# Optimization experiments

Measured on AMD Instinct MI355X. Metric: run time of the kernel, lower is better.

The kernel has to match this reference:

```python
import jax, jax.numpy as jnp
import numpy as np

DIM = 128
CODEBOOK_SCALE = 16384
N_TOKENS = 16384


def setup_inputs() -> dict:
    key = jax.random.key(0)
    k1, k2 = jax.random.split(key)
    x = jax.random.normal(k1, (N_TOKENS, DIM), dtype=jnp.float32)
    codebook = jax.random.normal(k2, (CODEBOOK_SCALE, DIM), dtype=jnp.float32)
    return {"x": x, "codebook": codebook}


def reference(x, codebook):
    # scores: [N, codebook_scale] = x @ codebook.T
    scores = jnp.einsum("nd,cd->nc", x, codebook)
    indices = jnp.argmax(scores, axis=-1)  # [N] int
    loss = jnp.zeros((), dtype=jnp.float32)  # original returns constant 0.0 loss
    return (indices, loss)
```

## Files before the change

kernel.cpp:

```cpp
#include <hip/hip_runtime.h>
#include <hip/hip_bf16.h>

#define NT 16384
#define ND 128
#define NC 16384
#define NSPLIT 8
#define MARGIN 0.4f
#define TILE_BYTES 16384
#define NTILES 32

typedef __bf16 bf16x8 __attribute__((ext_vector_type(8)));
typedef unsigned short u16x8 __attribute__((ext_vector_type(8)));
typedef float f32x4 __attribute__((ext_vector_type(4)));

#define MF __builtin_amdgcn_mfma_f32_16x16x32_bf16

static __device__ __forceinline__ unsigned short f2bf(float f) {
    unsigned u = __float_as_uint(f);
    return (unsigned short)((u + 0x7FFFu + ((u >> 16) & 1u)) >> 16);
}
static __device__ __forceinline__ float bf2f(unsigned short u) {
    return __uint_as_float(((unsigned)u) << 16);
}
static __device__ __forceinline__ bf16x8 u2b(u16x8 u) {
    return __builtin_bit_cast(bf16x8, u);
}
static __device__ __forceinline__ void gl2lds(const void* g, void* l) {
    __builtin_amdgcn_global_load_lds(
        (const __attribute__((address_space(1))) unsigned int*)g,
        (__attribute__((address_space(3))) unsigned int*)l, 16, 0, 0);
}

__global__ __launch_bounds__(512) void lfq_convert_cb(
    const float4* __restrict__ cb4, unsigned short* __restrict__ cbs)
{
    const unsigned i = blockIdx.x * 512 + threadIdx.x;
    float4 v = cb4[i];
    const unsigned c    = i >> 5;
    const unsigned d0   = (i & 31u) << 2;
    const unsigned tile = c >> 6, r = c & 63u;
    const unsigned pos  = ((d0 >> 3) + r) & 15u;
    const unsigned base = tile * 8192u + r * 128u + pos * 8u + (d0 & 7u);
    ushort4 h;
    h.x = f2bf(v.x);
    h.y = f2bf(v.y);
    h.z = f2bf(v.z);
    h.w = f2bf(v.w);
    *(ushort4*)(cbs + base) = h;
}

static __device__ __forceinline__ float exact_dot(
    const float4* __restrict__ xr4, const float* __restrict__ cf, int cidx)
{
    const float4* cr = (const float4*)(cf + (size_t)cidx * ND);
    float a0 = 0.f, a1 = 0.f, a2 = 0.f, a3 = 0.f;
#pragma unroll
    for (int i = 0; i < 32; i += 4) {
        float4 x0 = xr4[i+0], x1 = xr4[i+1], x2 = xr4[i+2], x3 = xr4[i+3];
        float4 c0 = cr[i+0],  c1 = cr[i+1],  c2 = cr[i+2],  c3 = cr[i+3];
        a0 += x0.x*c0.x + x0.y*c0.y + x0.z*c0.z + x0.w*c0.w;
        a1 += x1.x*c1.x + x1.y*c1.y + x1.z*c1.z + x1.w*c1.w;
        a2 += x2.x*c2.x + x2.y*c2.y + x2.z*c2.z + x2.w*c2.w;
        a3 += x3.x*c3.x + x3.y*c3.y + x3.z*c3.z + x3.w*c3.w;
    }
    return (a0 + a1) + (a2 + a3);
}

static __device__ __forceinline__ float exact_dot_g(
    const float* __restrict__ xf, const float* __restrict__ cf,
    int token, int cidx)
{
    const float4* xr = (const float4*)(xf + (size_t)token * ND);
    const float4* cr = (const float4*)(cf + (size_t)cidx * ND);
    float a0 = 0.f, a1 = 0.f, a2 = 0.f, a3 = 0.f;
#pragma unroll
    for (int i = 0; i < 32; i += 4) {
        float4 x0 = xr[i+0], x1 = xr[i+1], x2 = xr[i+2], x3 = xr[i+3];
        float4 c0 = cr[i+0], c1 = cr[i+1], c2 = cr[i+2], c3 = cr[i+3];
        a0 += x0.x*c0.x + x0.y*c0.y + x0.z*c0.z + x0.w*c0.w;
        a1 += x1.x*c1.x + x1.y*c1.y + x1.z*c1.z + x1.w*c1.w;
        a2 += x2.x*c2.x + x2.y*c2.y + x2.z*c2.z + x2.w*c2.w;
        a3 += x3.x*c3.x + x3.y*c3.y + x3.z*c3.z + x3.w*c3.w;
    }
    return (a0 + a1) + (a2 + a3);
}

static __device__ __forceinline__ void top2_upd(
    const f32x4& a, float* b1r, float* b2r, unsigned pk)
{
#pragma unroll
    for (int r4 = 0; r4 < 4; ++r4) {
        float p = __uint_as_float((__float_as_uint(a[r4]) & 0xFFFFFF80u) | pk);
        b2r[r4] = __builtin_amdgcn_fmed3f(p, b1r[r4], b2r[r4]);
        b1r[r4] = fmaxf(p, b1r[r4]);
    }
}

__global__ __launch_bounds__(256, 4) void lfq_stage1(
    const float* __restrict__ xf, const unsigned short* __restrict__ cbs,
    float* __restrict__ sb1, float* __restrict__ sb2,
    int* __restrict__ si1, int* __restrict__ si2)
{
    const int split = blockIdx.x & 7;
    const int tb    = blockIdx.x >> 3;
    const int t0    = tb * 128;
    const int tid   = threadIdx.x;
    const int w     = tid >> 6;
    const int lane  = tid & 63;
    const int n     = lane & 15;
    const int quad  = lane >> 4;

    __shared__ __attribute__((aligned(16))) unsigned char lds[2 * TILE_BYTES];

    bf16x8 ah[2][4];
#pragma unroll
    for (int tt = 0; tt < 2; ++tt) {
        const float* xr = xf + (size_t)(t0 + w * 32 + tt * 16 + n) * ND + quad * 8;
#pragma unroll
        for (int kk = 0; kk < 4; ++kk) {
            float4 v0 = *(const float4*)(xr + kk * 32);
            float4 v1 = *(const float4*)(xr + kk * 32 + 4);
            u16x8 hu;
            hu[0] = f2bf(v0.x);
            hu[1] = f2bf(v0.y);
            hu[2] = f2bf(v0.z);
            hu[3] = f2bf(v0.w);
            hu[4] = f2bf(v1.x);
            hu[5] = f2bf(v1.y);
            hu[6] = f2bf(v1.z);
            hu[7] = f2bf(v1.w);
            ah[tt][kk] = u2b(hu);
        }
    }

    float b1[2][4], b2[2][4];
#pragma unroll
    for (int tt = 0; tt < 2; ++tt)
#pragma unroll
        for (int r = 0; r < 4; ++r) { b1[tt][r] = -3.0e38f; b2[tt][r] = -3.0e38f; }

    const unsigned char* gtiles =
        (const unsigned char*)cbs + (size_t)(split * NTILES) * TILE_BYTES;
    const unsigned sgo  = (unsigned)(tid * 16);
    const unsigned ldso = (unsigned)(w * 1024);

    const unsigned bb0 = (unsigned)n * 256u + ((((unsigned)(quad + n     )) & 15u) << 4);
    const unsigned bb1 = (unsigned)n * 256u + ((((unsigned)(quad + n +  4)) & 15u) << 4);
    const unsigned bb2 = (unsigned)n * 256u + ((((unsigned)(quad + n +  8)) & 15u) << 4);
    const unsigned bb3 = (unsigned)n * 256u + ((((unsigned)(quad + n + 12)) & 15u) << 4);

    const f32x4 zq = {0.f, 0.f, 0.f, 0.f};

#pragma unroll
    for (int rd = 0; rd < 4; ++rd)
        gl2lds(gtiles + rd * 4096 + sgo, &lds[rd * 4096 + ldso]);
    __syncthreads();

#define PAIR(BUFO, SOFF, PKBASE)                                               \
    {                                                                          \
        bf16x8 qa0 = *(const bf16x8*)&lds[(BUFO) + (SOFF)          + bb0];     \
        bf16x8 qa1 = *(const bf16x8*)&lds[(BUFO) + (SOFF)          + bb1];     \
        bf16x8 qa2 = *(const bf16x8*)&lds[(BUFO) + (SOFF)          + bb2];     \
        bf16x8 qa3 = *(const bf16x8*)&lds[(BUFO) + (SOFF)          + bb3];     \
        bf16x8 qb0 = *(const bf16x8*)&lds[(BUFO) + (SOFF) + 4096u  + bb0];     \
        bf16x8 qb1 = *(const bf16x8*)&lds[(BUFO) + (SOFF) + 4096u  + bb1];     \
        bf16x8 qb2 = *(const bf16x8*)&lds[(BUFO) + (SOFF) + 4096u  + bb2];     \
        bf16x8 qb3 = *(const bf16x8*)&lds[(BUFO) + (SOFF) + 4096u  + bb3];     \
        f32x4 aA0, aA1, aB0, aB1;                                              \
        __builtin_amdgcn_s_setprio(1);                                         \
        aA0 = MF(ah[0][0], qa0, zq,  0,0,0);                                   \
        aA1 = MF(ah[1][0], qa0, zq,  0,0,0);                                   \
        aB0 = MF(ah[0][0], qb0, zq,  0,0,0);                                   \
        aB1 = MF(ah[1][0], qb0, zq,  0,0,0);                                   \
        aA0 = MF(ah[0][1], qa1, aA0, 0,0,0);                                   \
        aA1 = MF(ah[1][1], qa1, aA1, 0,0,0);                                   \
        aB0 = MF(ah[0][1], qb1, aB0, 0,0,0);                                   \
        aB1 = MF(ah[1][1], qb1, aB1, 0,0,0);                                   \
        aA0 = MF(ah[0][2], qa2, aA0, 0,0,0);                                   \
        aA1 = MF(ah[1][2], qa2, aA1, 0,0,0);                                   \
        aB0 = MF(ah[0][2], qb2, aB0, 0,0,0);                                   \
        aB1 = MF(ah[1][2], qb2, aB1, 0,0,0);                                   \
        aA0 = MF(ah[0][3], qa3, aA0, 0,0,0);                                   \
        aA1 = MF(ah[1][3], qa3, aA1, 0,0,0);                                   \
        aB0 = MF(ah[0][3], qb3, aB0, 0,0,0);                                   \
        aB1 = MF(ah[1][3], qb3, aB1, 0,0,0);                                   \
        __builtin_amdgcn_s_setprio(0);                                         \
        const unsigned pkA = (unsigned)(127 - (PKBASE));                       \
        const unsigned pkB = (unsigned)(127 - ((PKBASE) + 1));                 \
        top2_upd(aA0, b1[0], b2[0], pkA);                                      \
        top2_upd(aA1, b1[1], b2[1], pkA);                                      \
        top2_upd(aB0, b1[0], b2[0], pkB);                                      \
        top2_upd(aB1, b1[1], b2[1], pkB);                                      \
    }

#define TILE_BODY(T, BUFO, NBO, PREF)                                          \
    {                                                                          \
        if (PREF) {                                                            \
            const unsigned char* g = gtiles + (size_t)((T) + 1) * TILE_BYTES;  \
            gl2lds(g +     0 + sgo, &lds[(NBO)          + ldso]);              \
            gl2lds(g +  4096 + sgo, &lds[(NBO) +  4096u + ldso]);              \
            gl2lds(g +  8192 + sgo, &lds[(NBO) +  8192u + ldso]);              \
            gl2lds(g + 12288 + sgo, &lds[(NBO) + 12288u + ldso]);              \
        }                                                                      \
        PAIR(BUFO, 0u,    (T) * 4)                                             \
        PAIR(BUFO, 8192u, (T) * 4 + 2)                                         \
    }

    for (int t = 0; t < NTILES; t += 2) {
        TILE_BODY(t,     0u,         TILE_BYTES, 1)
        __syncthreads();
        TILE_BODY(t + 1, TILE_BYTES, 0u,         (t + 2 < NTILES))
        __syncthreads();
    }
#undef TILE_BODY
#undef PAIR

    const int cb_base = split * (NC / NSPLIT);
    float v1[2][4], v2[2][4];
    int   c1[2][4], c2[2][4];
#pragma unroll
    for (int tt = 0; tt < 2; ++tt)
#pragma unroll
        for (int r = 0; r < 4; ++r) {
            int j1 = 127 - (int)(__float_as_uint(b1[tt][r]) & 127u);
            int j2 = 127 - (int)(__float_as_uint(b2[tt][r]) & 127u);
            v1[tt][r] = b1[tt][r]; c1[tt][r] = cb_base + j1 * 16 + n;
            v2[tt][r] = b2[tt][r]; c2[tt][r] = cb_base + j2 * 16 + n;
        }

#pragma unroll
    for (int tt = 0; tt < 2; ++tt)
#pragma unroll
        for (int r = 0; r < 4; ++r) {
#pragma unroll
            for (int off = 1; off < 16; off <<= 1) {
                float ob1 = __shfl_xor(v1[tt][r], off, 64);
                int   oi1 = __shfl_xor(c1[tt][r], off, 64);
                float ob2 = __shfl_xor(v2[tt][r], off, 64);
                int   oi2 = __shfl_xor(c2[tt][r], off, 64);
                bool gt = (ob1 > v1[tt][r]) ||
                          (ob1 == v1[tt][r] && oi1 < c1[tt][r]);
                float ls = gt ? v1[tt][r] : ob1;
                int   li = gt ? c1[tt][r] : oi1;
                float ws_ = gt ? ob2 : v2[tt][r];
                int   wi = gt ? oi2 : c2[tt][r];
                bool s2 = (ls > ws_) || (ls == ws_ && li < wi);
                v2[tt][r] = s2 ? ls : ws_;
                c2[tt][r] = s2 ? li : wi;
                v1[tt][r] = gt ? ob1 : v1[tt][r];
                c1[tt][r] = gt ? oi1 : c1[tt][r];
            }
        }

    if (n == 0) {
#pragma unroll
        for (int tt = 0; tt < 2; ++tt)
#pragma unroll
            for (int r = 0; r < 4; ++r) {
                const int token = t0 + w * 32 + tt * 16 + quad * 4 + r;
                const size_t o = (size_t)split * NT + token;
                sb1[o] = v1[tt][r]; si1[o] = c1[tt][r];
                sb2[o] = v2[tt][r]; si2[o] = c2[tt][r];
            }
    }
}

__global__ __launch_bounds__(256) void lfq_combine(
    const float* __restrict__ sb1, const float* __restrict__ sb2,
    const int* __restrict__ si1, const int* __restrict__ si2,
    const float* __restrict__ xf, const float* __restrict__ cf,
    float* __restrict__ out, int out_size)
{
    const int lane = threadIdx.x & 63;
    const int wv   = threadIdx.x >> 6;
    const int g    = lane >> 3;
    const int cl   = lane & 7;
    const int t    = (blockIdx.x * 4 + wv) * 8 + g;

    const size_t o = (size_t)cl * NT + t;
    const float va = sb1[o]; const int ia = si1[o];
    const float vb = sb2[o]; const int ib = si2[o];

    bool lgt = (vb > va) || (vb == va && ib < ia);
    float m  = lgt ? vb : va;
    int   mi = lgt ? ib : ia;
#pragma unroll
    for (int off = 1; off < 8; off <<= 1) {
        float om = __shfl_xor(m, off, 64);
        int   oi = __shfl_xor(mi, off, 64);
        if (om > m || (om == m && oi < mi)) { m = om; mi = oi; }
    }
    const float A1 = m;
    const int   I1 = mi;

    const bool ba = (va >= A1 - MARGIN);
    const bool bb_ = (vb >= A1 - MARGIN);
    int cnt = (ba ? 1 : 0) + (bb_ ? 1 : 0);
#pragma unroll
    for (int off = 1; off < 8; off <<= 1)
        cnt += __shfl_xor(cnt, off, 64);

    int bi = I1;
    if (cnt > 1) {
        float sa = -__builtin_inff(), sb_ = -__builtin_inff();
        if (ba)  sa  = exact_dot_g(xf, cf, t, ia);
        if (bb_) sb_ = exact_dot_g(xf, cf, t, ib);
        bool g2 = (sb_ > sa) || (sb_ == sa && ib < ia);
        float bs = g2 ? sb_ : sa;
        int  bid = g2 ? ib : ia;
#pragma unroll
        for (int off = 1; off < 8; off <<= 1) {
            float os = __shfl_xor(bs, off, 64);
            int   oi = __shfl_xor(bid, off, 64);
            if (os > bs || (os == bs && oi < bid)) { bs = os; bid = oi; }
        }
        bi = bid;
    }
    if (cl == 0) out[t] = (float)bi;
    if (blockIdx.x == 0 && threadIdx.x == 0 && out_size > NT) out[NT] = 0.0f;
}

__global__ __launch_bounds__(512) void lfq_fp32_argmax(
    const float* __restrict__ xf, const float* __restrict__ cf,
    float* __restrict__ out, int out_size)
{
    const int tid = threadIdx.x;
    const int w   = tid >> 6;
    const int tok = tid & 63;
    const int t0  = blockIdx.x * 64;
    __shared__ float s_sc[8][64];
    __shared__ int   s_ix[8][64];

    float4 xr[32];
    const float4* xrow = (const float4*)(xf + (size_t)(t0 + tok) * ND);
#pragma unroll
    for (int i = 0; i < 32; ++i) xr[i] = xrow[i];

    float bs = -__builtin_inff();
    int   bi = 0;
    const int c_begin = w * (NC / 8);
    for (int c = c_begin; c < c_begin + NC / 8; ++c) {
        float s = exact_dot(xr, cf, c);
        if (s > bs) { bs = s; bi = c; }
    }
    s_sc[w][tok] = bs; s_ix[w][tok] = bi;
    __syncthreads();
    if (tid < 64) {
        float bsf = s_sc[0][tid]; int bif = s_ix[0][tid];
#pragma unroll
        for (int ww = 1; ww < 8; ++ww) {
            float s2 = s_sc[ww][tid]; int ii = s_ix[ww][tid];
            if (s2 > bsf || (s2 == bsf && ii < bif)) { bsf = s2; bif = ii; }
        }
        out[t0 + tid] = (float)bif;
    }
    if (blockIdx.x == 0 && tid == 0 && out_size > NT) out[NT] = 0.0f;
}

extern "C" void kernel_launch(void* const* d_in, const int* in_sizes, int n_in,
                              void* d_out, int out_size, void* d_ws, size_t ws_size,
                              hipStream_t stream) {
    const float* x  = (const float*)d_in[0];
    const float* cb = (const float*)d_in[1];
    float* out = (float*)d_out;

    const size_t NCE = (size_t)NC * ND;
    const size_t NEED = NCE * 2 + (size_t)NT * NSPLIT * 4 * 4;
    if (ws_size >= NEED) {
        char* ws = (char*)d_ws;
        unsigned short* cbs = (unsigned short*)ws;
        char* sp = ws + NCE * 2;
        float* sb1 = (float*)sp;
        float* sb2 = (float*)(sp + (size_t)NT * NSPLIT * 4);
        int*   si1 = (int*)  (sp + (size_t)NT * NSPLIT * 8);
        int*   si2 = (int*)  (sp + (size_t)NT * NSPLIT * 12);

        lfq_convert_cb<<<dim3(1024), dim3(512), 0, stream>>>(
            (const float4*)cb, cbs);
        lfq_stage1<<<dim3((NT / 128) * NSPLIT), dim3(256), 0, stream>>>(
            x, cbs, sb1, sb2, si1, si2);
        lfq_combine<<<dim3(NT / 32), dim3(256), 0, stream>>>(
            sb1, sb2, si1, si2, x, cb, out, out_size);
    } else {
        lfq_fp32_argmax<<<dim3(NT / 64), dim3(512), 0, stream>>>(x, cb, out, out_size);
    }
}
```

Baseline: 163.5 us.

## Double tokens per wave in stage1 and widen codebook conversion stores

Stage1 now gives each wave 64 tokens (4 A-fragments) instead of 32, so each codebook tile loaded into LDS is reused across twice as many MFMAs. This halves the LDS fill traffic per token and halves the grid to 512 blocks. It pins occupancy at 2 waves per EU to leave room for the larger register footprint. The convert kernel now has each thread handle 8 floats and write one 16-byte bf16 store, while keeping the same swizzled layout. The trade-off is fewer blocks and less latency hiding, plus higher register pressure.

```diff
diff --git a/kernel.cpp b/kernel.cpp
--- a/kernel.cpp
+++ b/kernel.cpp
@@ -31,22 +31,20 @@
         (__attribute__((address_space(3))) unsigned int*)l, 16, 0, 0);
 }
 
-__global__ __launch_bounds__(512) void lfq_convert_cb(
+__global__ __launch_bounds__(256) void lfq_convert_cb(
     const float4* __restrict__ cb4, unsigned short* __restrict__ cbs)
 {
-    const unsigned i = blockIdx.x * 512 + threadIdx.x;
-    float4 v = cb4[i];
-    const unsigned c    = i >> 5;
-    const unsigned d0   = (i & 31u) << 2;
+    const unsigned i = blockIdx.x * 256 + threadIdx.x;
+    const unsigned c = i >> 4;
+    const unsigned k = i & 15u;
+    const float4 v0 = cb4[i * 2];
+    const float4 v1 = cb4[i * 2 + 1];
     const unsigned tile = c >> 6, r = c & 63u;
-    const unsigned pos  = ((d0 >> 3) + r) & 15u;
-    const unsigned base = tile * 8192u + r * 128u + pos * 8u + (d0 & 7u);
-    ushort4 h;
-    h.x = f2bf(v.x);
-    h.y = f2bf(v.y);
-    h.z = f2bf(v.z);
-    h.w = f2bf(v.w);
-    *(ushort4*)(cbs + base) = h;
+    const unsigned pos  = (k + r) & 15u;
+    u16x8 h;
+    h[0] = f2bf(v0.x); h[1] = f2bf(v0.y); h[2] = f2bf(v0.z); h[3] = f2bf(v0.w);
+    h[4] = f2bf(v1.x); h[5] = f2bf(v1.y); h[6] = f2bf(v1.z); h[7] = f2bf(v1.w);
+    *(u16x8*)(cbs + tile * 8192u + r * 128u + pos * 8u) = h;
 }
 
 static __device__ __forceinline__ float exact_dot(
@@ -96,14 +94,16 @@
     }
 }
 
-__global__ __launch_bounds__(256, 4) void lfq_stage1(
+__global__ __launch_bounds__(256)
+__attribute__((amdgpu_waves_per_eu(2, 2)))
+void lfq_stage1(
     const float* __restrict__ xf, const unsigned short* __restrict__ cbs,
     float* __restrict__ sb1, float* __restrict__ sb2,
     int* __restrict__ si1, int* __restrict__ si2)
 {
     const int split = blockIdx.x & 7;
     const int tb    = blockIdx.x >> 3;
-    const int t0    = tb * 128;
+    const int t0    = tb * 256;
     const int tid   = threadIdx.x;
     const int w     = tid >> 6;
     const int lane  = tid & 63;
@@ -112,10 +112,10 @@
 
     __shared__ __attribute__((aligned(16))) unsigned char lds[2 * TILE_BYTES];
 
-    bf16x8 ah[2][4];
-#pragma unroll
-    for (int tt = 0; tt < 2; ++tt) {
-        const float* xr = xf + (size_t)(t0 + w * 32 + tt * 16 + n) * ND + quad * 8;
+    bf16x8 ah[4][4];
+#pragma unroll
+    for (int tt = 0; tt < 4; ++tt) {
+        const float* xr = xf + (size_t)(t0 + w * 64 + tt * 16 + n) * ND + quad * 8;
 #pragma unroll
         for (int kk = 0; kk < 4; ++kk) {
             float4 v0 = *(const float4*)(xr + kk * 32);
@@ -133,9 +133,9 @@
         }
     }
 
-    float b1[2][4], b2[2][4];
-#pragma unroll
-    for (int tt = 0; tt < 2; ++tt)
+    float b1[4][4], b2[4][4];
+#pragma unroll
+    for (int tt = 0; tt < 4; ++tt)
 #pragma unroll
         for (int r = 0; r < 4; ++r) { b1[tt][r] = -3.0e38f; b2[tt][r] = -3.0e38f; }
 
@@ -166,31 +166,51 @@
         bf16x8 qb1 = *(const bf16x8*)&lds[(BUFO) + (SOFF) + 4096u  + bb1];     \
         bf16x8 qb2 = *(const bf16x8*)&lds[(BUFO) + (SOFF) + 4096u  + bb2];     \
         bf16x8 qb3 = *(const bf16x8*)&lds[(BUFO) + (SOFF) + 4096u  + bb3];     \
-        f32x4 aA0, aA1, aB0, aB1;                                              \
+        f32x4 aA0, aA1, aA2, aA3, aB0, aB1, aB2, aB3;                          \
         __builtin_amdgcn_s_setprio(1);                                         \
         aA0 = MF(ah[0][0], qa0, zq,  0,0,0);                                   \
         aA1 = MF(ah[1][0], qa0, zq,  0,0,0);                                   \
+        aA2 = MF(ah[2][0], qa0, zq,  0,0,0);                                   \
+        aA3 = MF(ah[3][0], qa0, zq,  0,0,0);                                   \
         aB0 = MF(ah[0][0], qb0, zq,  0,0,0);                                   \
         aB1 = MF(ah[1][0], qb0, zq,  0,0,0);                                   \
+        aB2 = MF(ah[2][0], qb0, zq,  0,0,0);                                   \
+        aB3 = MF(ah[3][0], qb0, zq,  0,0,0);                                   \
         aA0 = MF(ah[0][1], qa1, aA0, 0,0,0);                                   \
         aA1 = MF(ah[1][1], qa1, aA1, 0,0,0);                                   \
+        aA2 = MF(ah[2][1], qa1, aA2, 0,0,0);                                   \
+        aA3 = MF(ah[3][1], qa1, aA3, 0,0,0);                                   \
         aB0 = MF(ah[0][1], qb1, aB0, 0,0,0);                                   \
         aB1 = MF(ah[1][1], qb1, aB1, 0,0,0);                                   \
+        aB2 = MF(ah[2][1], qb1, aB2, 0,0,0);                                   \
+        aB3 = MF(ah[3][1], qb1, aB3, 0,0,0);                                   \
         aA0 = MF(ah[0][2], qa2, aA0, 0,0,0);                                   \
         aA1 = MF(ah[1][2], qa2, aA1, 0,0,0);                                   \
+        aA2 = MF(ah[2][2], qa2, aA2, 0,0,0);                                   \
+        aA3 = MF(ah[3][2], qa2, aA3, 0,0,0);                                   \
         aB0 = MF(ah[0][2], qb2, aB0, 0,0,0);                                   \
         aB1 = MF(ah[1][2], qb2, aB1, 0,0,0);                                   \
+        aB2 = MF(ah[2][2], qb2, aB2, 0,0,0);                                   \
+        aB3 = MF(ah[3][2], qb2, aB3, 0,0,0);                                   \
         aA0 = MF(ah[0][3], qa3, aA0, 0,0,0);                                   \
         aA1 = MF(ah[1][3], qa3, aA1, 0,0,0);                                   \
+        aA2 = MF(ah[2][3], qa3, aA2, 0,0,0);                                   \
+        aA3 = MF(ah[3][3], qa3, aA3, 0,0,0);                                   \
         aB0 = MF(ah[0][3], qb3, aB0, 0,0,0);                                   \
         aB1 = MF(ah[1][3], qb3, aB1, 0,0,0);                                   \
+        aB2 = MF(ah[2][3], qb3, aB2, 0,0,0);                                   \
+        aB3 = MF(ah[3][3], qb3, aB3, 0,0,0);                                   \
         __builtin_amdgcn_s_setprio(0);                                         \
         const unsigned pkA = (unsigned)(127 - (PKBASE));                       \
         const unsigned pkB = (unsigned)(127 - ((PKBASE) + 1));                 \
         top2_upd(aA0, b1[0], b2[0], pkA);                                      \
         top2_upd(aA1, b1[1], b2[1], pkA);                                      \
+        top2_upd(aA2, b1[2], b2[2], pkA);                                      \
+        top2_upd(aA3, b1[3], b2[3], pkA);                                      \
         top2_upd(aB0, b1[0], b2[0], pkB);                                      \
         top2_upd(aB1, b1[1], b2[1], pkB);                                      \
+        top2_upd(aB2, b1[2], b2[2], pkB);                                      \
+        top2_upd(aB3, b1[3], b2[3], pkB);                                      \
     }
 
 #define TILE_BODY(T, BUFO, NBO, PREF)                                          \
@@ -216,10 +236,10 @@
 #undef PAIR
 
     const int cb_base = split * (NC / NSPLIT);
-    float v1[2][4], v2[2][4];
-    int   c1[2][4], c2[2][4];
-#pragma unroll
-    for (int tt = 0; tt < 2; ++tt)
+    float v1[4][4], v2[4][4];
+    int   c1[4][4], c2[4][4];
+#pragma unroll
+    for (int tt = 0; tt < 4; ++tt)
 #pragma unroll
         for (int r = 0; r < 4; ++r) {
             int j1 = 127 - (int)(__float_as_uint(b1[tt][r]) & 127u);
@@ -229,7 +249,7 @@
         }
 
 #pragma unroll
-    for (int tt = 0; tt < 2; ++tt)
+    for (int tt = 0; tt < 4; ++tt)
 #pragma unroll
         for (int r = 0; r < 4; ++r) {
 #pragma unroll
@@ -254,10 +274,10 @@
 
     if (n == 0) {
 #pragma unroll
-        for (int tt = 0; tt < 2; ++tt)
+        for (int tt = 0; tt < 4; ++tt)
 #pragma unroll
             for (int r = 0; r < 4; ++r) {
-                const int token = t0 + w * 32 + tt * 16 + quad * 4 + r;
+                const int token = t0 + w * 64 + tt * 16 + quad * 4 + r;
                 const size_t o = (size_t)split * NT + token;
                 sb1[o] = v1[tt][r]; si1[o] = c1[tt][r];
                 sb2[o] = v2[tt][r]; si2[o] = c2[tt][r];
@@ -375,9 +395,9 @@
         int*   si1 = (int*)  (sp + (size_t)NT * NSPLIT * 8);
         int*   si2 = (int*)  (sp + (size_t)NT * NSPLIT * 12);
 
-        lfq_convert_cb<<<dim3(1024), dim3(512), 0, stream>>>(
+        lfq_convert_cb<<<dim3(1024), dim3(256), 0, stream>>>(
             (const float4*)cb, cbs);
-        lfq_stage1<<<dim3((NT / 128) * NSPLIT), dim3(256), 0, stream>>>(
+        lfq_stage1<<<dim3((NT / 256) * NSPLIT), dim3(256), 0, stream>>>(
             x, cbs, sb1, sb2, si1, si2);
         lfq_combine<<<dim3(NT / 32), dim3(256), 0, stream>>>(
             sb1, sb2, si1, si2, x, cb, out, out_size);
```

Measured after the change: 161.9 us. About the same (-1.0%).
